# Kernel optimization log

Hardware: AMD Instinct MI355X
Metric: run time of the kernel (lower is better)

The kernel has to match this reference:

```python
import jax, jax.numpy as jnp
import numpy as np

DIM = 768
NUM_HEADS = 12
MAX_DIST = 32


def _build_relative_index(max_dist):
    # Faithful port of the torch buffer construction (pure numpy, static).
    ii, jj = np.meshgrid(np.arange(max_dist), np.arange(max_dist), indexing='ij')
    coords_flat = np.stack([ii.reshape(-1), jj.reshape(-1)], axis=0)  # [2, max_dist^2]
    rel = coords_flat[:, :, None] - coords_flat[:, None, :]          # [2, L, L]
    rel = rel.transpose(1, 2, 0) + (max_dist - 1)
    rel_index = rel[:, :, 0] * (2 * max_dist - 1) + rel[:, :, 1]
    return jnp.asarray(rel_index, dtype=jnp.int32)                   # [L, L]


def setup_inputs() -> dict:
    key = jax.random.key(0)
    k_x, k_qkv, k_proj, k_pb, k_bt = jax.random.split(key, 5)
    B, N, C = 8, 1024, DIM
    std = 0.02
    x = jax.random.normal(k_x, (B, N, C), dtype=jnp.float32)
    qkv_w = jax.random.normal(k_qkv, (C, 3 * C), dtype=jnp.float32) * std  # Linear(dim, 3*dim, bias=False)
    proj_w = jax.random.normal(k_proj, (C, C), dtype=jnp.float32) * std
    proj_b = jax.random.normal(k_pb, (C,), dtype=jnp.float32) * std
    bias_table = jax.random.normal(k_bt, ((2 * MAX_DIST - 1) ** 2, NUM_HEADS), dtype=jnp.float32) * std
    rel_index = _build_relative_index(MAX_DIST)
    return {"x": x, "qkv_w": qkv_w, "proj_w": proj_w, "proj_b": proj_b,
            "bias_table": bias_table, "rel_index": rel_index}


def reference(x, qkv_w, proj_w, proj_b, bias_table, rel_index):
    B, N, C = x.shape
    H = NUM_HEADS
    hd = C // H
    scale = hd ** -0.5
    qkv = (x @ qkv_w).reshape(B, N, 3, H, hd)
    q, k, v = qkv[:, :, 0], qkv[:, :, 1], qkv[:, :, 2]          # [B, N, H, hd]
    attn = jnp.einsum('bnhd,bmhd->bhnm', q, k) * scale           # [B, H, N, N]
    # gathered relative position bias, added per head before softmax
    rel_bias = bias_table[rel_index[:N, :N].reshape(-1)]         # [N*N, H]
    rel_bias = rel_bias.reshape(N, N, H).transpose(2, 0, 1)      # [H, N, N]
    attn = jax.nn.softmax(attn + rel_bias[None], axis=-1)
    out = jnp.einsum('bhnm,bmhd->bnhd', attn, v).reshape(B, N, C)
    return out @ proj_w + proj_b
```

## Files before the change

kernel.cpp:

```cpp
#include <hip/hip_runtime.h>
#include <hip/hip_bf16.h>
#include <stdint.h>

typedef unsigned short u16;
typedef __attribute__((ext_vector_type(8))) short short8;
typedef __attribute__((ext_vector_type(4))) short short4v;
typedef __attribute__((ext_vector_type(8))) __bf16 bf16x8;
typedef __attribute__((ext_vector_type(4))) float floatx4;

typedef const uint32_t __attribute__((address_space(1))) *gptr1;
typedef uint32_t __attribute__((address_space(3))) *lptr3;

#define DIMC 768
#define NH   12
#define HD   64
#define NB   8
#define SEQ  1024
#define MROWS (NB*SEQ)
#define BTAB_N 47628
#define PB_N   768
#define LOG2E 1.44269504088896340736f

__device__ __forceinline__ float bf2f(u16 u){ return __uint_as_float(((uint32_t)u)<<16); }
__device__ __forceinline__ u16 f2bf(float f){
  uint32_t u = __float_as_uint(f);
  u += 0x7fffu + ((u>>16)&1u);
  return (u16)(u>>16);
}
__device__ __forceinline__ uint32_t pack2(float lo, float hi){
  return (uint32_t)f2bf(lo) | ((uint32_t)f2bf(hi) << 16);
}
__device__ __forceinline__ floatx4 mfma16(short8 a, short8 b, floatx4 c){
  return __builtin_amdgcn_mfma_f32_16x16x32_bf16(
      __builtin_bit_cast(bf16x8, a), __builtin_bit_cast(bf16x8, b), c, 0, 0, 0);
}
__device__ __forceinline__ floatx4 mfma1k(short4v a, short4v b, floatx4 c){
  return __builtin_amdgcn_mfma_f32_16x16x16bf16_1k(a, b, c, 0, 0, 0);
}

__global__ __launch_bounds__(256) void detect_dtype(
    const u16* __restrict__ x, int* __restrict__ flag)
{
  __shared__ int cnt[256];
  int c = 0;
  for (int i = threadIdx.x; i < 2048; i += 256) {
    int e = (x[i] >> 7) & 0xFF;
    c += (e >= 0x8E);
  }
  cnt[threadIdx.x] = c;
  __syncthreads();
  for (int s = 128; s > 0; s >>= 1) {
    if ((int)threadIdx.x < s) cnt[threadIdx.x] += cnt[threadIdx.x + s];
    __syncthreads();
  }
  if (threadIdx.x == 0) *flag = (cnt[0] > 16) ? 1 : 0;
}

__global__ __launch_bounds__(256) void convert_x(
    const void* __restrict__ in, u16* __restrict__ outp,
    const int* __restrict__ flag, int n4)
{
  int idx = blockIdx.x * 256 + threadIdx.x;
  if (idx >= n4) return;
  ushort4 o;
  if (*flag) {
    const float4 v = ((const float4*)in)[idx];
    o.x = f2bf(v.x); o.y = f2bf(v.y); o.z = f2bf(v.z); o.w = f2bf(v.w);
  } else {
    o = ((const ushort4*)in)[idx];
  }
  ((ushort4*)outp)[idx] = o;
}

__global__ __launch_bounds__(256) void convert_small(
    const void* __restrict__ btab, const void* __restrict__ pb,
    u16* __restrict__ btabB, u16* __restrict__ pbB, const int* __restrict__ flag)
{
  int f = *flag;
  int idx = blockIdx.x * 256 + threadIdx.x;
  if (idx < BTAB_N) {
    float v = f ? ((const float*)btab)[idx] : bf2f(((const u16*)btab)[idx]);
    btabB[idx] = f2bf(v * LOG2E);
  } else if (idx < BTAB_N + PB_N) {
    int j = idx - BTAB_N;
    pbB[j] = f ? f2bf(((const float*)pb)[j]) : ((const u16*)pb)[j];
  }
}

__global__ __launch_bounds__(256) void transpose_any(
    const void* __restrict__ in, u16* __restrict__ out, int R, int C,
    const int* __restrict__ flag)
{
  __shared__ __align__(16) u16 t[64][65];
  const int f = *flag;
  const size_t bo = (size_t)blockIdx.z * R * C;
  const int r0 = blockIdx.y * 64, c0 = blockIdx.x * 64;
  const int tx = threadIdx.x & 63, ty = threadIdx.x >> 6;
  #pragma unroll
  for (int i = ty; i < 64; i += 4) {
    size_t src = bo + (size_t)(r0 + i) * C + c0 + tx;
    t[i][tx] = f ? f2bf(((const float*)in)[src]) : ((const u16*)in)[src];
  }
  __syncthreads();
  #pragma unroll
  for (int i = ty; i < 64; i += 4)
    out[bo + (size_t)(c0 + i) * R + r0 + tx] = t[tx][i];
}

__global__ __launch_bounds__(256) void build_bias(
    const int* __restrict__ rel, const u16* __restrict__ table, u16* __restrict__ biasM)
{
  const int t = blockIdx.x * 256 + threadIdx.x;
  const int idx = rel[t];
  const u16* row = table + idx * NH;
  #pragma unroll
  for (int h = 0; h < NH; ++h)
    biasM[(size_t)h * (SEQ * SEQ) + t] = row[h];
}

template<int MODE>
__global__ __launch_bounds__(256) void gemm_bt(
    const u16* __restrict__ A, const u16* __restrict__ Bt,
    int M, int N, int K,
    u16* __restrict__ Qb, u16* __restrict__ Kb, u16* __restrict__ Vt,
    float* __restrict__ Out, const u16* __restrict__ bias)
{
  __shared__ __align__(16) u16 As[128 * 64];
  __shared__ __align__(16) u16 Bs[128 * 64];
  const int m0 = blockIdx.x * 128, n0 = blockIdx.y * 128;
  const int tid = threadIdx.x;
  const int wave = tid >> 6, lane = tid & 63;
  const int wx = wave & 1, wy = wave >> 1;
  const int r15 = lane & 15, quad = lane >> 4;
  const int sw = r15 & 7;

  const floatx4 zf = {0.f, 0.f, 0.f, 0.f};
  floatx4 acc[4][4];
  #pragma unroll
  for (int i = 0; i < 4; ++i)
    #pragma unroll
    for (int j = 0; j < 4; ++j) acc[i][j] = zf;

  for (int kt = 0; kt < K; kt += 64) {
    __syncthreads();
    #pragma unroll
    for (int s = 0; s < 4; ++s) {
      int c = s * 256 + wave * 64 + lane;
      int row = c >> 3, cc = (c & 7) ^ (row & 7);
      __builtin_amdgcn_global_load_lds(
          (gptr1)(const void*)&A[(size_t)(m0 + row) * K + kt + cc * 8],
          (lptr3)(void*)&As[c * 8], 16, 0, 0);
      __builtin_amdgcn_global_load_lds(
          (gptr1)(const void*)&Bt[(size_t)(n0 + row) * K + kt + cc * 8],
          (lptr3)(void*)&Bs[c * 8], 16, 0, 0);
    }
    __syncthreads();
    #pragma unroll
    for (int ks = 0; ks < 64; ks += 32) {
      const int kc = ks >> 3;
      short8 a[4], b[4];
      #pragma unroll
      for (int i = 0; i < 4; ++i)
        a[i] = *(const short8*)&As[(wy * 64 + i * 16 + r15) * 64 + ((kc + quad) ^ sw) * 8];
      #pragma unroll
      for (int j = 0; j < 4; ++j)
        b[j] = *(const short8*)&Bs[(wx * 64 + j * 16 + r15) * 64 + ((kc + quad) ^ sw) * 8];
      #pragma unroll
      for (int i = 0; i < 4; ++i)
        #pragma unroll
        for (int j = 0; j < 4; ++j)
          acc[i][j] = mfma16(a[i], b[j], acc[i][j]);
    }
  }

  #pragma unroll
  for (int i = 0; i < 4; ++i)
    #pragma unroll
    for (int j = 0; j < 4; ++j)
      #pragma unroll
      for (int g = 0; g < 4; ++g) {
        int gm = m0 + wy * 64 + i * 16 + quad * 4 + g;
        int gn = n0 + wx * 64 + j * 16 + r15;
        float v = acc[i][j][g];
        if (MODE == 0) {
          int three = gn / DIMC;
          int hn = gn - three * DIMC;
          int h = hn >> 6, d = hn & 63;
          int b_ = gm >> 10, n = gm & 1023;
          int bh = b_ * NH + h;
          if (three == 0)      Qb[(((size_t)bh) * SEQ + n) * HD + d] = f2bf(v * (0.125f * LOG2E));
          else if (three == 1) Kb[(((size_t)bh) * SEQ + n) * HD + d] = f2bf(v);
          else                 Vt[(((size_t)bh) * HD + d) * SEQ + n] = f2bf(v);
        } else {
          Out[(size_t)gm * N + gn] = v + bf2f(bias[gn]);
        }
      }
}

template<int USEB>
__global__ __launch_bounds__(256, 6) void attention(
    const u16* __restrict__ Qb, const u16* __restrict__ Kb, const u16* __restrict__ Vt,
    const u16* __restrict__ biasB, u16* __restrict__ Ob)
{
  __shared__ __align__(16) u16 Qs[64 * 64];
  __shared__ __align__(16) u16 Ks[64 * 64];
  __shared__ __align__(16) u16 Vs[64 * 64];

  const int bh = blockIdx.x;
  const int h = bh % NH, b_ = bh / NH;
  const int q0 = blockIdx.y * 64;
  const int tid = threadIdx.x;
  const int wave = tid >> 6, lane = tid & 63;
  const int r15 = lane & 15, quad = lane >> 4;
  const int sw = r15 & 7;

  const u16* Qp = Qb + (size_t)bh * SEQ * HD;
  const u16* Kp = Kb + (size_t)bh * SEQ * HD;
  const u16* Vp = Vt + (size_t)bh * HD * SEQ;
  const u16* Bp = USEB ? (biasB + (size_t)h * SEQ * SEQ) : biasB;

  #pragma unroll
  for (int s = 0; s < 2; ++s) {
    int c = tid + s * 256;
    int row = c >> 3, cc = (c & 7) ^ (row & 7);
    *(int4*)&Qs[row * 64 + cc * 8] = *(const int4*)&Qp[(size_t)(q0 + row) * HD + (c & 7) * 8];
  }

  const int q = q0 + wave * 16 + r15;
  const size_t bqoff = (size_t)q * SEQ;
  const int qrow = wave * 16 + r15;

  const floatx4 zf = {0.f, 0.f, 0.f, 0.f};
  floatx4 o[4];
  #pragma unroll
  for (int Jm = 0; Jm < 4; ++Jm) o[Jm] = zf;
  float lpart = 0.f;

  for (int kt = 0; kt < 16; ++kt) {
    __syncthreads();
    #pragma unroll
    for (int s = 0; s < 2; ++s) {
      int c = tid + s * 256;
      int row = c >> 3, cc = (c & 7) ^ (row & 7);
      *(int4*)&Ks[row * 64 + cc * 8] = *(const int4*)&Kp[(size_t)(kt * 64 + row) * HD + (c & 7) * 8];
      *(int4*)&Vs[row * 64 + cc * 8] = *(const int4*)&Vp[(size_t)row * SEQ + kt * 64 + (c & 7) * 8];
    }
    __syncthreads();

    ushort4 bc[4];
    if (USEB) {
      #pragma unroll
      for (int Jk = 0; Jk < 4; ++Jk)
        bc[Jk] = *(const ushort4*)&Bp[bqoff + kt * 64 + Jk * 16 + quad * 4];
    }

    floatx4 sT[4];
    #pragma unroll
    for (int Jk = 0; Jk < 4; ++Jk) sT[Jk] = zf;

    #pragma unroll
    for (int ks = 0; ks < 64; ks += 32) {
      const int kc = ks >> 3;
      const short8 bq = *(const short8*)&Qs[qrow * 64 + ((kc + quad) ^ sw) * 8];
      #pragma unroll
      for (int Jk = 0; Jk < 4; ++Jk) {
        const short8 ak = *(const short8*)&Ks[(Jk * 16 + r15) * 64 + ((kc + quad) ^ sw) * 8];
        sT[Jk] = mfma16(ak, bq, sT[Jk]);
      }
    }

    #pragma unroll
    for (int Jk = 0; Jk < 4; ++Jk) {
      if (USEB) {
        sT[Jk][0] += bf2f(bc[Jk].x); sT[Jk][1] += bf2f(bc[Jk].y);
        sT[Jk][2] += bf2f(bc[Jk].z); sT[Jk][3] += bf2f(bc[Jk].w);
      } else {
        #pragma unroll
        for (int g = 0; g < 4; ++g) {
          const int k = kt * 64 + Jk * 16 + quad * 4 + g;
          const int idx = ((q >> 5) - (k >> 5) + 31) * 63 + ((q & 31) - (k & 31) + 31);
          sT[Jk][g] += bf2f(Bp[idx * NH + h]);
        }
      }
      const float p0 = exp2f(sT[Jk][0]);
      const float p1 = exp2f(sT[Jk][1]);
      const float p2v = exp2f(sT[Jk][2]);
      const float p3 = exp2f(sT[Jk][3]);
      lpart += (p0 + p1) + (p2v + p3);
      uint2 pw;
      pw.x = pack2(p0, p1);
      pw.y = pack2(p2v, p3);
      const short4v bp = __builtin_bit_cast(short4v, pw);
      const int vcol = ((2 * Jk + (quad >> 1)) ^ sw) * 8 + (quad & 1) * 4;
      #pragma unroll
      for (int Jm = 0; Jm < 4; ++Jm) {
        const short4v av = *(const short4v*)&Vs[(Jm * 16 + r15) * 64 + vcol];
        o[Jm] = mfma1k(av, bp, o[Jm]);
      }
    }
  }

  float l = lpart;
  l += __shfl_xor(l, 16, 64);
  l += __shfl_xor(l, 32, 64);
  const float inv = 1.0f / l;

  #pragma unroll
  for (int Jm = 0; Jm < 4; ++Jm) {
    ushort4 st;
    st.x = f2bf(o[Jm][0] * inv);
    st.y = f2bf(o[Jm][1] * inv);
    st.z = f2bf(o[Jm][2] * inv);
    st.w = f2bf(o[Jm][3] * inv);
    *(ushort4*)&Ob[((size_t)(b_ * SEQ + q)) * DIMC + h * HD + Jm * 16 + quad * 4] = st;
  }
}

extern "C" void kernel_launch(void* const* d_in, const int* in_sizes, int n_in,
                              void* d_out, int out_size, void* d_ws, size_t ws_size,
                              hipStream_t stream)
{
  (void)in_sizes; (void)n_in; (void)out_size;
  const void* x_raw  = d_in[0];
  const void* qkv_w  = d_in[1];
  const void* proj_w = d_in[2];
  const void* proj_b = d_in[3];
  const void* btab   = d_in[4];
  const int*  rel    = (const int*)d_in[5];
  float* out = (float*)d_out;

  const size_t SZ_FLAG = 256;
  const size_t SZ_XB   = (size_t)MROWS * DIMC * 2;
  const size_t SZ_BTAB = (BTAB_N * 2 + 255) & ~(size_t)255;
  const size_t SZ_PB   = (PB_N * 2 + 255) & ~(size_t)255;
  const size_t SZ_WQT  = (size_t)3 * DIMC * DIMC * 2;
  const size_t SZ_WPT  = (size_t)DIMC * DIMC * 2;
  const size_t SZ_T    = (size_t)NB * NH * SEQ * HD * 2;
  const size_t SZ_BM   = (size_t)NH * SEQ * SEQ * 2;
  const size_t NEED_FULL = SZ_FLAG + SZ_XB + SZ_BTAB + SZ_PB + SZ_WQT + SZ_WPT
                         + 3 * SZ_T + SZ_BM;

  char* p = (char*)d_ws;
  int* flag  = (int*)p;  p += SZ_FLAG;
  u16* xB    = (u16*)p;  p += SZ_XB;
  u16* btabB = (u16*)p;  p += SZ_BTAB;
  u16* pbB   = (u16*)p;  p += SZ_PB;
  u16* wqT   = (u16*)p;  p += SZ_WQT;
  u16* wpT   = (u16*)p;  p += SZ_WPT;
  u16* Qb    = (u16*)p;  p += SZ_T;
  u16* Kb    = (u16*)p;  p += SZ_T;
  u16* Vt    = (u16*)p;  p += SZ_T;
  u16* biasM = (u16*)p;

  const bool useBiasM = (ws_size >= NEED_FULL);
  const int n4 = MROWS * DIMC / 4;

  detect_dtype<<<1, 256, 0, stream>>>((const u16*)x_raw, flag);
  convert_x<<<(n4 + 255) / 256, 256, 0, stream>>>(x_raw, xB, flag, n4);
  convert_small<<<(BTAB_N + PB_N + 255) / 256, 256, 0, stream>>>(btab, proj_b, btabB, pbB, flag);
  transpose_any<<<dim3(3 * DIMC / 64, DIMC / 64, 1), 256, 0, stream>>>(qkv_w, wqT, DIMC, 3 * DIMC, flag);
  transpose_any<<<dim3(DIMC / 64, DIMC / 64, 1), 256, 0, stream>>>(proj_w, wpT, DIMC, DIMC, flag);
  gemm_bt<0><<<dim3(MROWS / 128, 3 * DIMC / 128), 256, 0, stream>>>(
      xB, wqT, MROWS, 3 * DIMC, DIMC, Qb, Kb, Vt, nullptr, nullptr);
  if (useBiasM) {
    build_bias<<<SEQ * SEQ / 256, 256, 0, stream>>>(rel, btabB, biasM);
    attention<1><<<dim3(NB * NH, SEQ / 64), 256, 0, stream>>>(Qb, Kb, Vt, biasM, xB);
  } else {
    attention<0><<<dim3(NB * NH, SEQ / 64), 256, 0, stream>>>(Qb, Kb, Vt, btabB, xB);
  }
  gemm_bt<1><<<dim3(MROWS / 128, DIMC / 128), 256, 0, stream>>>(
      xB, wpT, MROWS, DIMC, DIMC, nullptr, nullptr, nullptr, out, pbB);
}
```

Measured before the change: 262.2 us.

## Enlarge attention query tile, use direct global-to-LDS loads, smaller-M proj GEMM

The attention kernel now processes 128 queries per block with 512 threads, so each K/V tile loaded into shared memory is reused by twice as many query rows. K, V and Q tiles are fetched with global_load_lds (direct global-to-LDS DMA) instead of going through registers, and the bias loads are issued before the tile loads. The projection GEMM is split into its own kernel with 64-row tiles to increase block count, and also uses direct LDS loads. The risks are fewer attention blocks (768) with a higher register and LDS footprint per block, and less K/V overlap because the loads still complete behind one barrier per tile.

```diff
diff --git a/kernel.cpp b/kernel.cpp
--- a/kernel.cpp
+++ b/kernel.cpp
@@ -27,7 +27,7 @@
   u += 0x7fffu + ((u>>16)&1u);
   return (u16)(u>>16);
 }
-__device__ __forceinline__ uint32_t pack2(float lo, float hi){
+__device__ __forceinline__ uint32_t pkbf(float lo, float hi){
   return (uint32_t)f2bf(lo) | ((uint32_t)f2bf(hi) << 16);
 }
 __device__ __forceinline__ floatx4 mfma16(short8 a, short8 b, floatx4 c){
@@ -118,13 +118,11 @@
     biasM[(size_t)h * (SEQ * SEQ) + t] = row[h];
 }
 
-template<int MODE>
-__global__ __launch_bounds__(256) void gemm_bt(
+__global__ __launch_bounds__(256) void gemm_qkv(
     const u16* __restrict__ A, const u16* __restrict__ Bt,
-    int M, int N, int K,
-    u16* __restrict__ Qb, u16* __restrict__ Kb, u16* __restrict__ Vt,
-    float* __restrict__ Out, const u16* __restrict__ bias)
-{
+    u16* __restrict__ Qb, u16* __restrict__ Kb, u16* __restrict__ Vt)
+{
+  const int K = DIMC;
   __shared__ __align__(16) u16 As[128 * 64];
   __shared__ __align__(16) u16 Bs[128 * 64];
   const int m0 = blockIdx.x * 128, n0 = blockIdx.y * 128;
@@ -182,33 +180,99 @@
         int gm = m0 + wy * 64 + i * 16 + quad * 4 + g;
         int gn = n0 + wx * 64 + j * 16 + r15;
         float v = acc[i][j][g];
-        if (MODE == 0) {
-          int three = gn / DIMC;
-          int hn = gn - three * DIMC;
-          int h = hn >> 6, d = hn & 63;
-          int b_ = gm >> 10, n = gm & 1023;
-          int bh = b_ * NH + h;
-          if (three == 0)      Qb[(((size_t)bh) * SEQ + n) * HD + d] = f2bf(v * (0.125f * LOG2E));
-          else if (three == 1) Kb[(((size_t)bh) * SEQ + n) * HD + d] = f2bf(v);
-          else                 Vt[(((size_t)bh) * HD + d) * SEQ + n] = f2bf(v);
-        } else {
-          Out[(size_t)gm * N + gn] = v + bf2f(bias[gn]);
-        }
+        int three = gn / DIMC;
+        int hn = gn - three * DIMC;
+        int h = hn >> 6, d = hn & 63;
+        int b_ = gm >> 10, n = gm & 1023;
+        int bh = b_ * NH + h;
+        if (three == 0)      Qb[(((size_t)bh) * SEQ + n) * HD + d] = f2bf(v * (0.125f * LOG2E));
+        else if (three == 1) Kb[(((size_t)bh) * SEQ + n) * HD + d] = f2bf(v);
+        else                 Vt[(((size_t)bh) * HD + d) * SEQ + n] = f2bf(v);
       }
 }
 
+__global__ __launch_bounds__(256) void gemm_proj(
+    const u16* __restrict__ A, const u16* __restrict__ Bt,
+    float* __restrict__ Out, const u16* __restrict__ bias)
+{
+  const int K = DIMC, N = DIMC;
+  __shared__ __align__(16) u16 As[64 * 64];
+  __shared__ __align__(16) u16 Bs[128 * 64];
+  const int m0 = blockIdx.x * 64, n0 = blockIdx.y * 128;
+  const int tid = threadIdx.x;
+  const int wave = tid >> 6, lane = tid & 63;
+  const int wy = wave >> 1, wx = wave & 1;
+  const int r15 = lane & 15, quad = lane >> 4;
+  const int sw = r15 & 7;
+
+  const floatx4 zf = {0.f, 0.f, 0.f, 0.f};
+  floatx4 acc[2][4];
+  #pragma unroll
+  for (int i = 0; i < 2; ++i)
+    #pragma unroll
+    for (int j = 0; j < 4; ++j) acc[i][j] = zf;
+
+  for (int kt = 0; kt < K; kt += 64) {
+    __syncthreads();
+    #pragma unroll
+    for (int s = 0; s < 2; ++s) {
+      int c = tid + s * 256;
+      int row = c >> 3, cc = (c & 7) ^ (row & 7);
+      __builtin_amdgcn_global_load_lds(
+          (gptr1)(const void*)&A[(size_t)(m0 + row) * K + kt + cc * 8],
+          (lptr3)(void*)&As[c * 8], 16, 0, 0);
+    }
+    #pragma unroll
+    for (int s = 0; s < 4; ++s) {
+      int c = tid + s * 256;
+      int row = c >> 3, cc = (c & 7) ^ (row & 7);
+      __builtin_amdgcn_global_load_lds(
+          (gptr1)(const void*)&Bt[(size_t)(n0 + row) * K + kt + cc * 8],
+          (lptr3)(void*)&Bs[c * 8], 16, 0, 0);
+    }
+    __syncthreads();
+    #pragma unroll
+    for (int ks = 0; ks < 64; ks += 32) {
+      const int kc = ks >> 3;
+      short8 a[2], b[4];
+      #pragma unroll
+      for (int i = 0; i < 2; ++i)
+        a[i] = *(const short8*)&As[(wy * 32 + i * 16 + r15) * 64 + ((kc + quad) ^ sw) * 8];
+      #pragma unroll
+      for (int j = 0; j < 4; ++j)
+        b[j] = *(const short8*)&Bs[(wx * 64 + j * 16 + r15) * 64 + ((kc + quad) ^ sw) * 8];
+      #pragma unroll
+      for (int i = 0; i < 2; ++i)
+        #pragma unroll
+        for (int j = 0; j < 4; ++j)
+          acc[i][j] = mfma16(a[i], b[j], acc[i][j]);
+    }
+  }
+
+  #pragma unroll
+  for (int i = 0; i < 2; ++i)
+    #pragma unroll
+    for (int j = 0; j < 4; ++j)
+      #pragma unroll
+      for (int g = 0; g < 4; ++g) {
+        int gm = m0 + wy * 32 + i * 16 + quad * 4 + g;
+        int gn = n0 + wx * 64 + j * 16 + r15;
+        Out[(size_t)gm * N + gn] = acc[i][j][g] + bf2f(bias[gn]);
+      }
+}
+
 template<int USEB>
-__global__ __launch_bounds__(256, 6) void attention(
+__global__ __launch_bounds__(512, 6) void attention(
     const u16* __restrict__ Qb, const u16* __restrict__ Kb, const u16* __restrict__ Vt,
     const u16* __restrict__ biasB, u16* __restrict__ Ob)
 {
-  __shared__ __align__(16) u16 Qs[64 * 64];
+  __shared__ __align__(16) u16 Qs[128 * 64];
   __shared__ __align__(16) u16 Ks[64 * 64];
   __shared__ __align__(16) u16 Vs[64 * 64];
 
   const int bh = blockIdx.x;
   const int h = bh % NH, b_ = bh / NH;
-  const int q0 = blockIdx.y * 64;
+  const int q0 = blockIdx.y * 128;
   const int tid = threadIdx.x;
   const int wave = tid >> 6, lane = tid & 63;
   const int r15 = lane & 15, quad = lane >> 4;
@@ -221,9 +285,11 @@
 
   #pragma unroll
   for (int s = 0; s < 2; ++s) {
-    int c = tid + s * 256;
+    int c = tid + s * 512;
     int row = c >> 3, cc = (c & 7) ^ (row & 7);
-    *(int4*)&Qs[row * 64 + cc * 8] = *(const int4*)&Qp[(size_t)(q0 + row) * HD + (c & 7) * 8];
+    __builtin_amdgcn_global_load_lds(
+        (gptr1)(const void*)&Qp[(size_t)(q0 + row) * HD + cc * 8],
+        (lptr3)(void*)&Qs[c * 8], 16, 0, 0);
   }
 
   const int q = q0 + wave * 16 + r15;
@@ -238,21 +304,23 @@
 
   for (int kt = 0; kt < 16; ++kt) {
     __syncthreads();
-    #pragma unroll
-    for (int s = 0; s < 2; ++s) {
-      int c = tid + s * 256;
-      int row = c >> 3, cc = (c & 7) ^ (row & 7);
-      *(int4*)&Ks[row * 64 + cc * 8] = *(const int4*)&Kp[(size_t)(kt * 64 + row) * HD + (c & 7) * 8];
-      *(int4*)&Vs[row * 64 + cc * 8] = *(const int4*)&Vp[(size_t)row * SEQ + kt * 64 + (c & 7) * 8];
-    }
-    __syncthreads();
-
     ushort4 bc[4];
     if (USEB) {
       #pragma unroll
       for (int Jk = 0; Jk < 4; ++Jk)
         bc[Jk] = *(const ushort4*)&Bp[bqoff + kt * 64 + Jk * 16 + quad * 4];
     }
+    {
+      int c = tid;
+      int row = c >> 3, cc = (c & 7) ^ (row & 7);
+      __builtin_amdgcn_global_load_lds(
+          (gptr1)(const void*)&Kp[(size_t)(kt * 64 + row) * HD + cc * 8],
+          (lptr3)(void*)&Ks[c * 8], 16, 0, 0);
+      __builtin_amdgcn_global_load_lds(
+          (gptr1)(const void*)&Vp[(size_t)row * SEQ + kt * 64 + cc * 8],
+          (lptr3)(void*)&Vs[c * 8], 16, 0, 0);
+    }
+    __syncthreads();
 
     floatx4 sT[4];
     #pragma unroll
@@ -288,8 +356,8 @@
       const float p3 = exp2f(sT[Jk][3]);
       lpart += (p0 + p1) + (p2v + p3);
       uint2 pw;
-      pw.x = pack2(p0, p1);
-      pw.y = pack2(p2v, p3);
+      pw.x = pkbf(p0, p1);
+      pw.y = pkbf(p2v, p3);
       const short4v bp = __builtin_bit_cast(short4v, pw);
       const int vcol = ((2 * Jk + (quad >> 1)) ^ sw) * 8 + (quad & 1) * 4;
       #pragma unroll
@@ -307,12 +375,10 @@
 
   #pragma unroll
   for (int Jm = 0; Jm < 4; ++Jm) {
-    ushort4 st;
-    st.x = f2bf(o[Jm][0] * inv);
-    st.y = f2bf(o[Jm][1] * inv);
-    st.z = f2bf(o[Jm][2] * inv);
-    st.w = f2bf(o[Jm][3] * inv);
-    *(ushort4*)&Ob[((size_t)(b_ * SEQ + q)) * DIMC + h * HD + Jm * 16 + quad * 4] = st;
+    uint2 st;
+    st.x = pkbf(o[Jm][0] * inv, o[Jm][1] * inv);
+    st.y = pkbf(o[Jm][2] * inv, o[Jm][3] * inv);
+    *(uint2*)&Ob[((size_t)(b_ * SEQ + q)) * DIMC + h * HD + Jm * 16 + quad * 4] = st;
   }
 }
 
@@ -360,14 +426,14 @@
   convert_small<<<(BTAB_N + PB_N + 255) / 256, 256, 0, stream>>>(btab, proj_b, btabB, pbB, flag);
   transpose_any<<<dim3(3 * DIMC / 64, DIMC / 64, 1), 256, 0, stream>>>(qkv_w, wqT, DIMC, 3 * DIMC, flag);
   transpose_any<<<dim3(DIMC / 64, DIMC / 64, 1), 256, 0, stream>>>(proj_w, wpT, DIMC, DIMC, flag);
-  gemm_bt<0><<<dim3(MROWS / 128, 3 * DIMC / 128), 256, 0, stream>>>(
-      xB, wqT, MROWS, 3 * DIMC, DIMC, Qb, Kb, Vt, nullptr, nullptr);
+  gemm_qkv<<<dim3(MROWS / 128, 3 * DIMC / 128), 256, 0, stream>>>(
+      xB, wqT, Qb, Kb, Vt);
   if (useBiasM) {
     build_bias<<<SEQ * SEQ / 256, 256, 0, stream>>>(rel, btabB, biasM);
-    attention<1><<<dim3(NB * NH, SEQ / 64), 256, 0, stream>>>(Qb, Kb, Vt, biasM, xB);
+    attention<1><<<dim3(NB * NH, SEQ / 128), 512, 0, stream>>>(Qb, Kb, Vt, biasM, xB);
   } else {
-    attention<0><<<dim3(NB * NH, SEQ / 64), 256, 0, stream>>>(Qb, Kb, Vt, btabB, xB);
-  }
-  gemm_bt<1><<<dim3(MROWS / 128, DIMC / 128), 256, 0, stream>>>(
-      xB, wpT, MROWS, DIMC, DIMC, nullptr, nullptr, nullptr, out, pbB);
-}
+    attention<0><<<dim3(NB * NH, SEQ / 128), 512, 0, stream>>>(Qb, Kb, Vt, btabB, xB);
+  }
+  gemm_proj<<<dim3(MROWS / 64, DIMC / 128), 256, 0, stream>>>(
+      xB, wpT, out, pbB);
+}
```

New measurement: 268.9 us. 1.03x slower.
